# Kernel optimization log

Measured on AMD Instinct MI355X. Metric: run time of the kernel, lower is better.

Reference implementation:

```python
import jax, jax.numpy as jnp
import numpy as np

MARGIN = 1.0
RULE_WEIGHT = 0.5
NUM_ENT = 100000
NUM_REL = 500
DIM = 512
N_RULES = 20


def setup_inputs() -> dict:
    key = jax.random.key(0)
    ks = jax.random.split(key, 8)
    pos_triples = jax.random.randint(ks[0], (1024, 3), 0, NUM_REL)
    neg_triples = jax.random.randint(ks[1], (8192, 3), 0, NUM_REL)
    rule_r1 = jax.random.randint(ks[2], (N_RULES,), 0, NUM_REL)
    rule_r2 = jax.random.randint(ks[3], (N_RULES,), 0, NUM_REL)
    rule_conf = jax.random.uniform(ks[4], (N_RULES,), dtype=jnp.float32)
    ent_emb = jax.random.normal(ks[5], (NUM_ENT, DIM), dtype=jnp.float32)
    rel_emb = jax.random.normal(ks[6], (NUM_REL, DIM), dtype=jnp.float32)
    norm_vec = jax.random.normal(ks[7], (NUM_REL, DIM), dtype=jnp.float32)
    return {
        "pos_triples": pos_triples, "neg_triples": neg_triples,
        "rule_r1": rule_r1, "rule_r2": rule_r2, "rule_conf": rule_conf,
        "ent_emb": ent_emb, "rel_emb": rel_emb, "norm_vec": norm_vec,
    }


def _transh_dist(h_idx, r_idx, t_idx, ent_emb, rel_emb, norm_vec):
    """TransH distance ||proj(h) + r - proj(t)||_2.
    Index args may have any broadcast-compatible shape; returns that shape."""
    w = norm_vec[r_idx]                                   # [..., d]
    w = w / jnp.linalg.norm(w, axis=-1, keepdims=True)
    he = ent_emb[h_idx]
    te = ent_emb[t_idx]
    re = rel_emb[r_idx]
    hp = he - jnp.sum(he * w, axis=-1, keepdims=True) * w  # hyperplane projection
    tp = te - jnp.sum(te * w, axis=-1, keepdims=True) * w
    return jnp.linalg.norm(hp + re - tp, axis=-1)


def reference(pos_triples, neg_triples, rule_r1, rule_r2, rule_conf,
              ent_emb, rel_emb, norm_vec):
    B = pos_triples.shape[0]
    neg_ratio = neg_triples.shape[0] // B
    # basic margin ranking loss: pos triples repeat-interleaved to align with negs
    exp_pos = jnp.repeat(pos_triples, neg_ratio, axis=0)   # [B*ratio, 3]
    d_pos = _transh_dist(exp_pos[:, 0], exp_pos[:, 1], exp_pos[:, 2],
                         ent_emb, rel_emb, norm_vec)
    d_neg = _transh_dist(neg_triples[:, 0], neg_triples[:, 1], neg_triples[:, 2],
                         ent_emb, rel_emb, norm_vec)
    basic_loss = jnp.mean(jax.nn.relu(MARGIN + d_pos - d_neg))

    # rule loss: for each pos triple i and rule j with r_i == r1_j,
    # rule_loss -= conf_j * score(h_i, r2_j, t_i), score = -distance.
    h = pos_triples[:, 0][:, None]        # [B,1]
    r = pos_triples[:, 1][:, None]        # [B,1]
    t = pos_triples[:, 2][:, None]        # [B,1]
    d_rule = _transh_dist(h, rule_r2[None, :], t, ent_emb, rel_emb, norm_vec)  # [B,nR]
    score = -d_rule
    mask = (r == rule_r1[None, :]).astype(score.dtype)     # [B,nR]
    rule_loss = -jnp.sum(mask * rule_conf[None, :] * score)

    return basic_loss + RULE_WEIGHT * rule_loss
```

## Files before the change

kernel.cpp:

```cpp
#include <hip/hip_runtime.h>

#define DIM        512
#define B_POS      1024
#define N_NEG      8192
#define N_RULES    20
#define NEG_RATIO  8

#define T_NEG   (B_POS)
#define T_RULE  (B_POS + N_NEG)
#define N_TASK  (T_RULE + B_POS * N_RULES)

__device__ __forceinline__ float wave_sum(float x) {
#pragma unroll
    for (int off = 32; off > 0; off >>= 1)
        x += __shfl_xor(x, off, 64);
    return x;
}

__device__ __forceinline__ float transh_dist(
    int h, int r, int t,
    const float* __restrict__ ent, const float* __restrict__ rel,
    const float* __restrict__ nv, int lane)
{
    const float4* wp = (const float4*)(nv  + (size_t)r * DIM);
    const float4* hp = (const float4*)(ent + (size_t)h * DIM);
    const float4* tp = (const float4*)(ent + (size_t)t * DIM);
    const float4* rp = (const float4*)(rel + (size_t)r * DIM);

    float4 wv[2], dv[2], rv[2];
    float ww = 0.f, dw = 0.f;
#pragma unroll
    for (int c = 0; c < 2; ++c) {
        float4 w  = wp[lane + 64 * c];
        float4 hh = hp[lane + 64 * c];
        float4 tt = tp[lane + 64 * c];
        float4 rr = rp[lane + 64 * c];
        float4 d;
        d.x = hh.x - tt.x; d.y = hh.y - tt.y; d.z = hh.z - tt.z; d.w = hh.w - tt.w;
        wv[c] = w; dv[c] = d; rv[c] = rr;
        ww += w.x * w.x + w.y * w.y + w.z * w.z + w.w * w.w;
        dw += d.x * w.x + d.y * w.y + d.z * w.z + d.w * w.w;
    }
    ww = wave_sum(ww);
    dw = wave_sum(dw);
    float s = dw / ww;

    float ss = 0.f;
#pragma unroll
    for (int c = 0; c < 2; ++c) {
        float vx = dv[c].x + rv[c].x - s * wv[c].x;
        float vy = dv[c].y + rv[c].y - s * wv[c].y;
        float vz = dv[c].z + rv[c].z - s * wv[c].z;
        float vw = dv[c].w + rv[c].w - s * wv[c].w;
        ss += vx * vx + vy * vy + vz * vz + vw * vw;
    }
    ss = wave_sum(ss);
    return sqrtf(ss);
}

__global__ __launch_bounds__(256) void dist_kernel(
    const int* __restrict__ pos, const int* __restrict__ neg,
    const int* __restrict__ rule_r1, const int* __restrict__ rule_r2,
    const float* __restrict__ rule_conf,
    const float* __restrict__ ent, const float* __restrict__ rel,
    const float* __restrict__ nv,
    float* __restrict__ dpos, float* __restrict__ dneg,
    float* __restrict__ rule_acc)
{
    int wid  = (int)((blockIdx.x * blockDim.x + threadIdx.x) >> 6);
    int lane = threadIdx.x & 63;
    if (wid >= N_TASK) return;

    if (wid < T_NEG) {
        int i = wid;
        int h = pos[3 * i], r = pos[3 * i + 1], t = pos[3 * i + 2];
        float d = transh_dist(h, r, t, ent, rel, nv, lane);
        if (lane == 0) dpos[i] = d;
    } else if (wid < T_RULE) {
        int i = wid - T_NEG;
        int h = neg[3 * i], r = neg[3 * i + 1], t = neg[3 * i + 2];
        float d = transh_dist(h, r, t, ent, rel, nv, lane);
        if (lane == 0) dneg[i] = d;
    } else {
        int p = wid - T_RULE;
        int i = p / N_RULES;
        int j = p - i * N_RULES;
        if (pos[3 * i + 1] != rule_r1[j]) return;
        int h = pos[3 * i], t = pos[3 * i + 2];
        int r2 = rule_r2[j];
        float d = transh_dist(h, r2, t, ent, rel, nv, lane);
        if (lane == 0) atomicAdd(rule_acc, rule_conf[j] * d);
    }
}

__global__ __launch_bounds__(256) void reduce_kernel(
    const float* __restrict__ dpos, const float* __restrict__ dneg,
    const float* __restrict__ rule_acc, float* __restrict__ out)
{
    float s = 0.f;
    for (int k = threadIdx.x; k < N_NEG; k += 256) {
        float v = 1.0f + dpos[k >> 3] - dneg[k];
        s += (v > 0.f) ? v : 0.f;
    }
    s = wave_sum(s);
    __shared__ float part[4];
    int w = threadIdx.x >> 6, lane = threadIdx.x & 63;
    if (lane == 0) part[w] = s;
    __syncthreads();
    if (threadIdx.x == 0) {
        float tot = part[0] + part[1] + part[2] + part[3];
        out[0] = tot / (float)N_NEG + 0.5f * rule_acc[0];
    }
}

extern "C" void kernel_launch(void* const* d_in, const int* in_sizes, int n_in,
                              void* d_out, int out_size, void* d_ws, size_t ws_size,
                              hipStream_t stream) {
    const int*   pos       = (const int*)  d_in[0];
    const int*   neg       = (const int*)  d_in[1];
    const int*   rule_r1   = (const int*)  d_in[2];
    const int*   rule_r2   = (const int*)  d_in[3];
    const float* rule_conf = (const float*)d_in[4];
    const float* ent       = (const float*)d_in[5];
    const float* rel       = (const float*)d_in[6];
    const float* nv        = (const float*)d_in[7];
    float* out = (float*)d_out;

    float* rule_acc = (float*)d_ws;
    float* dpos     = rule_acc + 16;
    float* dneg     = dpos + B_POS;

    hipMemsetAsync(d_ws, 0, 64, stream);

    int nblocks = (N_TASK + 3) / 4;
    dist_kernel<<<nblocks, 256, 0, stream>>>(pos, neg, rule_r1, rule_r2, rule_conf,
                                             ent, rel, nv, dpos, dneg, rule_acc);
    reduce_kernel<<<1, 256, 0, stream>>>(dpos, dneg, rule_acc, out);
}
```

Baseline: 259.3 us.

## Fuse margin loss and rule loss into per-positive-triple waves with block partials

Each wave now handles one positive triple: it computes the positive distance, its 8 negatives with the ReLU margin inline, and the matching rules in a loop. Block partials are written to workspace and summed by a tiny final kernel. This removes the memset, the atomics, the dpos/dneg round trip and the launch of about 28K mostly-idle rule waves. In exchange the grid drops to 256 blocks (1024 waves) with serial work per wave, which lowers parallelism and latency hiding on a GPU with many CUs.

```diff
diff --git a/kernel.cpp b/kernel.cpp
--- a/kernel.cpp
+++ b/kernel.cpp
@@ -5,10 +5,7 @@
 #define N_NEG      8192
 #define N_RULES    20
 #define NEG_RATIO  8
-
-#define T_NEG   (B_POS)
-#define T_RULE  (B_POS + N_NEG)
-#define N_TASK  (T_RULE + B_POS * N_RULES)
+#define NBLK       256
 
 __device__ __forceinline__ float wave_sum(float x) {
 #pragma unroll
@@ -58,59 +55,58 @@
     return sqrtf(ss);
 }
 
-__global__ __launch_bounds__(256) void dist_kernel(
+__global__ __launch_bounds__(256) void fused_kernel(
     const int* __restrict__ pos, const int* __restrict__ neg,
     const int* __restrict__ rule_r1, const int* __restrict__ rule_r2,
     const float* __restrict__ rule_conf,
     const float* __restrict__ ent, const float* __restrict__ rel,
     const float* __restrict__ nv,
-    float* __restrict__ dpos, float* __restrict__ dneg,
-    float* __restrict__ rule_acc)
+    float* __restrict__ partial)
 {
-    int wid  = (int)((blockIdx.x * blockDim.x + threadIdx.x) >> 6);
+    int w    = threadIdx.x >> 6;
     int lane = threadIdx.x & 63;
-    if (wid >= N_TASK) return;
+    int i    = blockIdx.x * 4 + w;
 
-    if (wid < T_NEG) {
-        int i = wid;
-        int h = pos[3 * i], r = pos[3 * i + 1], t = pos[3 * i + 2];
-        float d = transh_dist(h, r, t, ent, rel, nv, lane);
-        if (lane == 0) dpos[i] = d;
-    } else if (wid < T_RULE) {
-        int i = wid - T_NEG;
-        int h = neg[3 * i], r = neg[3 * i + 1], t = neg[3 * i + 2];
-        float d = transh_dist(h, r, t, ent, rel, nv, lane);
-        if (lane == 0) dneg[i] = d;
-    } else {
-        int p = wid - T_RULE;
-        int i = p / N_RULES;
-        int j = p - i * N_RULES;
-        if (pos[3 * i + 1] != rule_r1[j]) return;
-        int h = pos[3 * i], t = pos[3 * i + 2];
-        int r2 = rule_r2[j];
-        float d = transh_dist(h, r2, t, ent, rel, nv, lane);
-        if (lane == 0) atomicAdd(rule_acc, rule_conf[j] * d);
+    int h = pos[3 * i], r = pos[3 * i + 1], t = pos[3 * i + 2];
+    float dp = transh_dist(h, r, t, ent, rel, nv, lane);
+
+    float relu_sum = 0.f;
+#pragma unroll
+    for (int k = 0; k < NEG_RATIO; ++k) {
+        int n = NEG_RATIO * i + k;
+        float dn = transh_dist(neg[3 * n], neg[3 * n + 1], neg[3 * n + 2],
+                               ent, rel, nv, lane);
+        float v = 1.0f + dp - dn;
+        relu_sum += (v > 0.f) ? v : 0.f;
     }
+
+    float rule_acc = 0.f;
+    for (int j = 0; j < N_RULES; ++j) {
+        if (r == rule_r1[j]) {
+            float d = transh_dist(h, rule_r2[j], t, ent, rel, nv, lane);
+            rule_acc += rule_conf[j] * d;
+        }
+    }
+
+    float contrib = relu_sum * (1.0f / (float)N_NEG) + 0.5f * rule_acc;
+
+    __shared__ float part[4];
+    if (lane == 0) part[w] = contrib;
+    __syncthreads();
+    if (threadIdx.x == 0)
+        partial[blockIdx.x] = part[0] + part[1] + part[2] + part[3];
 }
 
-__global__ __launch_bounds__(256) void reduce_kernel(
-    const float* __restrict__ dpos, const float* __restrict__ dneg,
-    const float* __restrict__ rule_acc, float* __restrict__ out)
+__global__ __launch_bounds__(64) void final_reduce(
+    const float* __restrict__ partial, float* __restrict__ out)
 {
+    int lane = threadIdx.x;
     float s = 0.f;
-    for (int k = threadIdx.x; k < N_NEG; k += 256) {
-        float v = 1.0f + dpos[k >> 3] - dneg[k];
-        s += (v > 0.f) ? v : 0.f;
-    }
+#pragma unroll
+    for (int m = 0; m < NBLK / 64; ++m)
+        s += partial[lane + 64 * m];
     s = wave_sum(s);
-    __shared__ float part[4];
-    int w = threadIdx.x >> 6, lane = threadIdx.x & 63;
-    if (lane == 0) part[w] = s;
-    __syncthreads();
-    if (threadIdx.x == 0) {
-        float tot = part[0] + part[1] + part[2] + part[3];
-        out[0] = tot / (float)N_NEG + 0.5f * rule_acc[0];
-    }
+    if (lane == 0) out[0] = s;
 }
 
 extern "C" void kernel_launch(void* const* d_in, const int* in_sizes, int n_in,
@@ -124,16 +120,10 @@
     const float* ent       = (const float*)d_in[5];
     const float* rel       = (const float*)d_in[6];
     const float* nv        = (const float*)d_in[7];
-    float* out = (float*)d_out;
+    float* out     = (float*)d_out;
+    float* partial = (float*)d_ws;
 
-    float* rule_acc = (float*)d_ws;
-    float* dpos     = rule_acc + 16;
-    float* dneg     = dpos + B_POS;
-
-    hipMemsetAsync(d_ws, 0, 64, stream);
-
-    int nblocks = (N_TASK + 3) / 4;
-    dist_kernel<<<nblocks, 256, 0, stream>>>(pos, neg, rule_r1, rule_r2, rule_conf,
-                                             ent, rel, nv, dpos, dneg, rule_acc);
-    reduce_kernel<<<1, 256, 0, stream>>>(dpos, dneg, rule_acc, out);
+    fused_kernel<<<NBLK, 256, 0, stream>>>(pos, neg, rule_r1, rule_r2, rule_conf,
+                                           ent, rel, nv, partial);
+    final_reduce<<<1, 64, 0, stream>>>(partial, out);
 }
```

Result: faster. 252.8 us (-2.5%).
